# Kernel optimization log

Measured on AMD Instinct MI355X. Metric: run time of the kernel, lower is better.

The kernel has to match this reference:

```python
import jax, jax.numpy as jnp
import numpy as np

B, D, H, W = 16, 64, 64, 64
K = 1024


def setup_inputs() -> dict:
    key = jax.random.key(0)
    k1, k2 = jax.random.split(key)
    x = jax.random.normal(k1, (B, D, H, W), dtype=jnp.float32)
    limit = 3.0 ** 0.5
    e_i_ts = jax.random.uniform(k2, (D, K), dtype=jnp.float32, minval=-limit, maxval=limit)
    return {"x": x, "e_i_ts": e_i_ts}


def reference(x, e_i_ts):
    b, d, h, w = x.shape
    # [B,H,W,D] -> [N,D]
    flat_x = jnp.transpose(x, (0, 2, 3, 1)).reshape(-1, d)
    distances = (
        jnp.sum(flat_x * flat_x, axis=1, keepdims=True)
        - 2.0 * (flat_x @ e_i_ts)
        + jnp.sum(e_i_ts * e_i_ts, axis=0, keepdims=True)
    )
    encoding_indices = jnp.argmin(distances, axis=1)  # [N]
    reshaped_indices = encoding_indices.reshape(b, h, w)
    # codebook gather: e_i_ts.T is [K,D]
    quantized = jnp.take(e_i_ts.T, reshaped_indices, axis=0)  # [B,H,W,D]
    quantized_x = jnp.transpose(quantized, (0, 3, 1, 2))  # [B,D,H,W]

    dictionary_loss = jnp.mean((jax.lax.stop_gradient(x) - quantized_x) ** 2)
    commitment_loss = jnp.mean((x - jax.lax.stop_gradient(quantized_x)) ** 2)
    # straight-through estimator
    quantized_x = x + jax.lax.stop_gradient(quantized_x - x)
    return quantized_x, dictionary_loss, commitment_loss, encoding_indices.reshape(b, -1)
```

## Files before the change

### kernel.cpp

```cpp
#include <hip/hip_runtime.h>

#define DD 64
#define KK 1024
#define NPTS 65536
#define TOTAL 4194304

#define OFF_L1 4194304
#define OFF_L2 4194305
#define OFF_IDX 4194306

#define WS_ENH_F 64
#define WS_EHT_BYTE 65536
#define WS_ELT_BYTE (65536 + 131072)

#define MARGIN_S 0.008f

typedef __attribute__((ext_vector_type(8))) short short8;
typedef __attribute__((ext_vector_type(4))) float f32x4;

__device__ __forceinline__ unsigned short bf16_rne(float f) {
    unsigned b = __float_as_uint(f);
    return (unsigned short)((b + 0x7FFFu + ((b >> 16) & 1u)) >> 16);
}
__device__ __forceinline__ float bf16_to_f(unsigned short h) {
    return __uint_as_float(((unsigned)h) << 16);
}
__device__ __forceinline__ unsigned umax(unsigned a, unsigned b) { return a > b ? a : b; }
__device__ __forceinline__ unsigned umin(unsigned a, unsigned b) { return a < b ? a : b; }
__device__ __forceinline__ void gld_lds16(const void* g, void* l) {
    __builtin_amdgcn_global_load_lds(
        (const __attribute__((address_space(1))) void*)g,
        (__attribute__((address_space(3))) void*)l, 16, 0, 0);
}
__device__ __forceinline__ int swz(int r, int d) {
    return ((d & ~7) ^ ((r & 7) << 3)) | (d & 7);
}

__global__ __launch_bounds__(256) void prep_kernel(const float* __restrict__ e,
                                                   float* __restrict__ enh,
                                                   unsigned short* __restrict__ ehT,
                                                   unsigned short* __restrict__ elT,
                                                   float* __restrict__ sum,
                                                   unsigned* __restrict__ tick) {
    __shared__ unsigned short tH[64 * 64];
    __shared__ unsigned short tL[64 * 64];
    __shared__ float ps[4 * 64];
    const int tid = threadIdx.x, wave = tid >> 6, lane = tid & 63;
    if (blockIdx.x == 0 && tid == 0) { *sum = 0.f; *tick = 0u; }
    const int k = blockIdx.x * 64 + lane;
    float s2 = 0.f;
    short8 hh[2], ll[2];
#pragma unroll
    for (int g = 0; g < 2; ++g)
#pragma unroll
        for (int j = 0; j < 8; ++j) {
            const int d = wave * 16 + g * 8 + j;
            const float v = e[d * KK + k];
            const unsigned short h = bf16_rne(v);
            hh[g][j] = (short)h;
            ll[g][j] = (short)bf16_rne(v - bf16_to_f(h));
            s2 = fmaf(v, v, s2);
        }
    ps[wave * 64 + lane] = s2;
#pragma unroll
    for (int g = 0; g < 2; ++g) {
        const int pos = lane * 64 + ((wave * 16 + g * 8) ^ ((k & 7) << 3));
        *(short8*)(tH + pos) = hh[g];
        *(short8*)(tL + pos) = ll[g];
    }
    __syncthreads();
    if (wave == 0) {
        const float t = ps[lane] + ps[64 + lane] + ps[128 + lane] + ps[192 + lane];
        enh[k] = 512.0f - 0.5f * t;
    }
    {
        const short8* srcH = (const short8*)tH;
        const short8* srcL = (const short8*)tL;
        short8* dstH = (short8*)(ehT + blockIdx.x * 64 * 64);
        short8* dstL = (short8*)(elT + blockIdx.x * 64 * 64);
        dstH[tid * 2]     = srcH[tid * 2];
        dstH[tid * 2 + 1] = srcH[tid * 2 + 1];
        dstL[tid * 2]     = srcL[tid * 2];
        dstL[tid * 2 + 1] = srcL[tid * 2 + 1];
    }
}

__global__ __launch_bounds__(256) void vq_gemm(const float* __restrict__ x,
                                               const float* __restrict__ e,
                                               const float* __restrict__ enh,
                                               const unsigned short* __restrict__ ehT,
                                               const unsigned short* __restrict__ elT,
                                               float* __restrict__ out,
                                               float* __restrict__ sum,
                                               unsigned* __restrict__ tick) {
    __shared__ __align__(16) char ebuf[2 * 16384];

    unsigned short* xbh = (unsigned short*)ebuf;
    unsigned short* xbl = (unsigned short*)(ebuf + 16384);
    int*   ks  = (int*)ebuf;
    float* xp  = (float*)(ks + 128);
    int*   rl  = (int*)(xp + 64);
    int*   rn  = rl + 128;
    float* rv  = (float*)(rn + 1);
    int*   ri  = (int*)(rv + 4);
    float* red = (float*)(ri + 4);

    const int tid = threadIdx.x;
    const int wave = tid >> 6, lane = tid & 63;
    const int n0 = blockIdx.x * 128;
    const int b = n0 >> 12;
    const int hw0 = n0 & 4095;

    const char* ehTb = (const char*)ehT;
    const char* elTb = (const char*)elT;
    const int lofs = wave * 1024 + lane * 16;

    {
        const int p = tid & 127, dg = tid >> 7;
        const float* xs = x + ((b * DD + dg * 32) << 12) + hw0 + p;
        float xv[32];
#pragma unroll
        for (int s = 0; s < 32; ++s) xv[s] = xs[s << 12];
#pragma unroll
        for (int g = 0; g < 4; ++g) {
            short8 hh, ll;
#pragma unroll
            for (int j = 0; j < 8; ++j) {
                const float f = xv[g * 8 + j];
                const unsigned short h = bf16_rne(f);
                hh[j] = (short)h;
                ll[j] = (short)bf16_rne(f - bf16_to_f(h));
            }
            const int d0 = dg * 32 + g * 8;
            const int pos = p * 64 + (d0 ^ ((p & 7) << 3));
            *(short8*)(xbh + pos) = hh;
            *(short8*)(xbl + pos) = ll;
        }
    }
    __syncthreads();

    const int ln15 = lane & 15, q8 = (lane >> 4) * 8;
    const int wp = wave * 32;

    short8 ah[2][2], al[2][2];
#pragma unroll
    for (int rf = 0; rf < 2; ++rf)
#pragma unroll
        for (int kc = 0; kc < 2; ++kc) {
            const int pp = wp + rf * 16 + ln15;
            const int pos = pp * 64 + ((kc * 32 + q8) ^ ((pp & 7) << 3));
            ah[rf][kc] = *(const short8*)(xbh + pos);
            al[rf][kc] = *(const short8*)(xbl + pos);
        }
    __syncthreads();

    {
        char* db = ebuf;
        gld_lds16(ehTb + lofs,        db + wave * 1024);
        gld_lds16(ehTb + 4096 + lofs, db + 4096 + wave * 1024);
        gld_lds16(elTb + lofs,        db + 8192 + wave * 1024);
        gld_lds16(elTb + 4096 + lofs, db + 12288 + wave * 1024);
    }

    unsigned v1u[8], v2u[8];
#pragma unroll
    for (int r = 0; r < 8; ++r) { v1u[r] = 0u; v2u[r] = 0u; }

    for (int kt = 0; kt < 16; ++kt) {
        __syncthreads();
        if (kt < 15) {
            const int nkt = kt + 1;
            char* db = ebuf + (nkt & 1) * 16384;
            const char* sH = ehTb + nkt * 8192 + lofs;
            const char* sL = elTb + nkt * 8192 + lofs;
            gld_lds16(sH,        db + wave * 1024);
            gld_lds16(sH + 4096, db + 4096 + wave * 1024);
            gld_lds16(sL,        db + 8192 + wave * 1024);
            gld_lds16(sL + 4096, db + 12288 + wave * 1024);
        }
        const unsigned short* ebH = (const unsigned short*)(ebuf + (kt & 1) * 16384);
        const unsigned short* ebL = ebH + 4096;

        f32x4 acc[2][4];
#pragma unroll
        for (int cf = 0; cf < 4; ++cf) {
            const float ec = enh[kt * 64 + cf * 16 + ln15];
#pragma unroll
            for (int rf = 0; rf < 2; ++rf)
                acc[rf][cf] = (f32x4){ec, ec, ec, ec};
        }

#pragma unroll
        for (int kc = 0; kc < 2; ++kc) {
            short8 bh[4], bl[4];
#pragma unroll
            for (int cf = 0; cf < 4; ++cf) {
                const int c = cf * 16 + ln15;
                const int pos = c * 64 + ((kc * 32 + q8) ^ ((c & 7) << 3));
                bh[cf] = *(const short8*)(ebH + pos);
                bl[cf] = *(const short8*)(ebL + pos);
            }
#pragma unroll
            for (int rf = 0; rf < 2; ++rf)
#pragma unroll
                for (int cf = 0; cf < 4; ++cf) {
                    acc[rf][cf] = __builtin_amdgcn_mfma_f32_16x16x32_bf16(al[rf][kc], bh[cf], acc[rf][cf], 0, 0, 0);
                    acc[rf][cf] = __builtin_amdgcn_mfma_f32_16x16x32_bf16(ah[rf][kc], bl[cf], acc[rf][cf], 0, 0, 0);
                    acc[rf][cf] = __builtin_amdgcn_mfma_f32_16x16x32_bf16(ah[rf][kc], bh[cf], acc[rf][cf], 0, 0, 0);
                }
        }

#pragma unroll
        for (int rf = 0; rf < 2; ++rf)
#pragma unroll
            for (int reg = 0; reg < 4; ++reg) {
                const int r = rf * 4 + reg;
                const unsigned k0 = (__float_as_uint(acc[rf][0][reg]) | 63u) ^ (unsigned)(kt * 4 + 0);
                const unsigned k1 = (__float_as_uint(acc[rf][1][reg]) | 63u) ^ (unsigned)(kt * 4 + 1);
                const unsigned k2 = (__float_as_uint(acc[rf][2][reg]) | 63u) ^ (unsigned)(kt * 4 + 2);
                const unsigned k3 = (__float_as_uint(acc[rf][3][reg]) | 63u) ^ (unsigned)(kt * 4 + 3);
                unsigned a = umax(k0, k1), bb = umin(k0, k1);
                v2u[r] = umax(umax(v2u[r], umin(v1u[r], a)), bb);
                v1u[r] = umax(v1u[r], a);
                a = umax(k2, k3); bb = umin(k2, k3);
                v2u[r] = umax(umax(v2u[r], umin(v1u[r], a)), bb);
                v1u[r] = umax(v1u[r], a);
            }
    }

    __syncthreads();
    if (tid == 0) *rn = 0;
    __syncthreads();

#pragma unroll
    for (int r = 0; r < 8; ++r) {
        const unsigned c6 = 63u - (v1u[r] & 63u);
        int col = (int)(c6 >> 2) * 64 + (int)(c6 & 3) * 16 + ln15;
        float val = __uint_as_float(v1u[r] & ~63u);
        float sec = __uint_as_float(v2u[r] & ~63u);
#pragma unroll
        for (int msk = 1; msk < 16; msk <<= 1) {
            const float ov = __shfl_xor(val, msk);
            const int oc = __shfl_xor(col, msk);
            const float os = __shfl_xor(sec, msk);
            sec = fmaxf(fmaxf(sec, os), fminf(val, ov));
            const bool t = (ov > val) || (ov == val && oc < col);
            val = t ? ov : val;
            col = t ? oc : col;
        }
        if (ln15 == 0) {
            const int qq = lane >> 4;
            const int pt = wp + (r >> 2) * 16 + qq * 4 + (r & 3);
            ks[pt] = col;
            if (val - sec < MARGIN_S) {
                const int w = atomicAdd(rn, 1);
                rl[w] = pt;
            }
        }
    }
    __syncthreads();

    const int lcnt = *rn;
    for (int it = 0; it < lcnt; ++it) {
        const int pr = rl[it];
        if (tid < 64) xp[tid] = x[((b * DD + tid) << 12) + hw0 + pr];
        __syncthreads();
        float d0 = 0.f, d1 = 0.f, d2 = 0.f, d3 = 0.f;
#pragma unroll 8
        for (int dd = 0; dd < DD; ++dd) {
            const float xd = xp[dd];
            const float4 ev = *(const float4*)(e + dd * KK + tid * 4);
            d0 = fmaf(xd, ev.x, d0);
            d1 = fmaf(xd, ev.y, d1);
            d2 = fmaf(xd, ev.z, d2);
            d3 = fmaf(xd, ev.w, d3);
        }
        const float4 ea = *(const float4*)(enh + tid * 4);
        float bs = d0 + ea.x;
        int bi2 = tid * 4;
        if (d1 + ea.y > bs) { bs = d1 + ea.y; bi2 = tid * 4 + 1; }
        if (d2 + ea.z > bs) { bs = d2 + ea.z; bi2 = tid * 4 + 2; }
        if (d3 + ea.w > bs) { bs = d3 + ea.w; bi2 = tid * 4 + 3; }
#pragma unroll
        for (int m = 1; m < 64; m <<= 1) {
            const float ov = __shfl_xor(bs, m, 64);
            const int oi = __shfl_xor(bi2, m, 64);
            if (ov > bs || (ov == bs && oi < bi2)) { bs = ov; bi2 = oi; }
        }
        if (lane == 0) { rv[wave] = bs; ri[wave] = bi2; }
        __syncthreads();
        if (tid == 0) {
            float gs = rv[0];
            int gi = ri[0];
#pragma unroll
            for (int t2 = 1; t2 < 4; ++t2)
                if (rv[t2] > gs || (rv[t2] == gs && ri[t2] < gi)) { gs = rv[t2]; gi = ri[t2]; }
            ks[pr] = gi;
        }
        __syncthreads();
    }

    if (tid < 128) out[OFF_IDX + n0 + tid] = (float)ks[tid];

    {
        const int pe = tid & 127, dh = tid >> 7;
        const int kp = ks[pe];
        float lacc = 0.f;
#pragma unroll
        for (int s = 0; s < 32; ++s) {
            const int d = dh * 32 + s;
            const float qv = e[d * KK + kp];
            const float xv = x[((b * DD + d) << 12) + hw0 + pe];
            out[((b * DD + d) << 12) + hw0 + pe] = qv;
            const float df = xv - qv;
            lacc = fmaf(df, df, lacc);
        }
#pragma unroll
        for (int off = 32; off > 0; off >>= 1) lacc += __shfl_down(lacc, off, 64);
        if (lane == 0) red[wave] = lacc;
    }
    __syncthreads();
    if (tid == 0) {
        atomicAdd(sum, red[0] + red[1] + red[2] + red[3]);
        __threadfence();
        const unsigned old = atomicAdd(tick, 1u);
        if (old == (unsigned)(gridDim.x - 1)) {
            const float s = atomicAdd(sum, 0.0f);
            const float m = s * (1.0f / (float)TOTAL);
            out[OFF_L1] = m;
            out[OFF_L2] = m;
        }
    }
}

extern "C" void kernel_launch(void* const* d_in, const int* in_sizes, int n_in,
                              void* d_out, int out_size, void* d_ws, size_t ws_size,
                              hipStream_t stream) {
    const float* x = (const float*)d_in[0];
    const float* e = (const float*)d_in[1];
    float* out = (float*)d_out;

    float* sum = (float*)d_ws;
    unsigned* tick = (unsigned*)d_ws + 2;
    float* enh = (float*)d_ws + WS_ENH_F;
    unsigned short* ehT = (unsigned short*)((char*)d_ws + WS_EHT_BYTE);
    unsigned short* elT = (unsigned short*)((char*)d_ws + WS_ELT_BYTE);

    prep_kernel<<<KK / 64, 256, 0, stream>>>(e, enh, ehT, elT, sum, tick);
    vq_gemm<<<NPTS / 128, 256, 0, stream>>>(x, e, enh, ehT, elT, out, sum, tick);
}
```

Measured before the change: 125.5 us.

## Split VQ GEMM into two launches with a triple-buffered per-wave codebook pipeline

The single 512-block launch becomes two 256-block launches. The first half of the points runs the original kernel. The second half runs a new variant where each wave streams its own codebook tiles into a three-slot LDS ring with async global-to-LDS loads and explicit vmcnt waits, and the codebook norms are cached in LDS. The aim is to overlap codebook loads with MFMA work. The cost is an extra kernel launch and serialization between the halves, and the completion counter now uses a fixed total of 512 blocks.

```diff
diff --git a/kernel.cpp b/kernel.cpp
--- a/kernel.cpp
+++ b/kernel.cpp
@@ -4,6 +4,7 @@
 #define KK 1024
 #define NPTS 65536
 #define TOTAL 4194304
+#define NBLK_TOTAL 512
 
 #define OFF_L1 4194304
 #define OFF_L2 4194305
@@ -85,14 +86,15 @@
     }
 }
 
-__global__ __launch_bounds__(256) void vq_gemm(const float* __restrict__ x,
-                                               const float* __restrict__ e,
-                                               const float* __restrict__ enh,
-                                               const unsigned short* __restrict__ ehT,
-                                               const unsigned short* __restrict__ elT,
-                                               float* __restrict__ out,
-                                               float* __restrict__ sum,
-                                               unsigned* __restrict__ tick) {
+
+__global__ __launch_bounds__(256) void vq_gemm_a(const float* __restrict__ x,
+                                                 const float* __restrict__ e,
+                                                 const float* __restrict__ enh,
+                                                 const unsigned short* __restrict__ ehT,
+                                                 const unsigned short* __restrict__ elT,
+                                                 float* __restrict__ out,
+                                                 float* __restrict__ sum,
+                                                 unsigned* __restrict__ tick) {
     __shared__ __align__(16) char ebuf[2 * 16384];
 
     unsigned short* xbh = (unsigned short*)ebuf;
@@ -324,7 +326,247 @@
         atomicAdd(sum, red[0] + red[1] + red[2] + red[3]);
         __threadfence();
         const unsigned old = atomicAdd(tick, 1u);
-        if (old == (unsigned)(gridDim.x - 1)) {
+        if (old == (unsigned)(NBLK_TOTAL - 1)) {
+            const float s = atomicAdd(sum, 0.0f);
+            const float m = s * (1.0f / (float)TOTAL);
+            out[OFF_L1] = m;
+            out[OFF_L2] = m;
+        }
+    }
+}
+
+__global__ __launch_bounds__(256) void vq_gemm_b(const float* __restrict__ x,
+                                                 const float* __restrict__ e,
+                                                 const float* __restrict__ enh,
+                                                 const unsigned short* __restrict__ ehT,
+                                                 const unsigned short* __restrict__ elT,
+                                                 float* __restrict__ out,
+                                                 float* __restrict__ sum,
+                                                 unsigned* __restrict__ tick) {
+    __shared__ __align__(16) char ebuf[4 * 12288];
+    __shared__ float enh_lds[1024];
+
+    unsigned short* xbh = (unsigned short*)ebuf;
+    unsigned short* xbl = (unsigned short*)(ebuf + 16384);
+    int*   ks  = (int*)ebuf;
+    float* xp  = (float*)(ks + 128);
+    int*   rl  = (int*)(xp + 64);
+    int*   rn  = rl + 128;
+    float* rv  = (float*)(rn + 1);
+    int*   ri  = (int*)(rv + 4);
+    float* red = (float*)(ri + 4);
+
+    const int tid = threadIdx.x;
+    const int wave = tid >> 6, lane = tid & 63;
+    const int n0 = (blockIdx.x + 256) * 128;
+    const int b = n0 >> 12;
+    const int hw0 = n0 & 4095;
+
+    const char* ehTb = (const char*)ehT;
+    const char* elTb = (const char*)elT;
+
+    *(float4*)(enh_lds + tid * 4) = *(const float4*)(enh + tid * 4);
+
+    {
+        const int p = tid & 127, dg = tid >> 7;
+        const float* xs = x + ((b * DD + dg * 32) << 12) + hw0 + p;
+        float xv[32];
+#pragma unroll
+        for (int s = 0; s < 32; ++s) xv[s] = xs[s << 12];
+#pragma unroll
+        for (int g = 0; g < 4; ++g) {
+            short8 hh, ll;
+#pragma unroll
+            for (int j = 0; j < 8; ++j) {
+                const float f = xv[g * 8 + j];
+                const unsigned short h = bf16_rne(f);
+                hh[j] = (short)h;
+                ll[j] = (short)bf16_rne(f - bf16_to_f(h));
+            }
+            const int d0 = dg * 32 + g * 8;
+            const int pos = p * 64 + (d0 ^ ((p & 7) << 3));
+            *(short8*)(xbh + pos) = hh;
+            *(short8*)(xbl + pos) = ll;
+        }
+    }
+    __syncthreads();
+
+    const int ln15 = lane & 15, q8 = (lane >> 4) * 8;
+    const int wp = wave * 32;
+
+    short8 ah[2][2], al[2][2];
+#pragma unroll
+    for (int rf = 0; rf < 2; ++rf)
+#pragma unroll
+        for (int kc = 0; kc < 2; ++kc) {
+            const int pp = wp + rf * 16 + ln15;
+            const int pos = pp * 64 + ((kc * 32 + q8) ^ ((pp & 7) << 3));
+            ah[rf][kc] = *(const short8*)(xbh + pos);
+            al[rf][kc] = *(const short8*)(xbl + pos);
+        }
+    __syncthreads();
+
+    char* wbuf = ebuf + wave * 12288;
+    char* r0 = wbuf;
+    char* r1 = wbuf + 4096;
+    char* r2 = wbuf + 8192;
+    const char* sHb = ehTb + lane * 16;
+    const char* sLb = elTb + lane * 16;
+
+#define ISSUE_B(t, dst)                                        \
+    {                                                          \
+        const char* sH = sHb + (t) * 2048;                     \
+        const char* sL = sLb + (t) * 2048;                     \
+        gld_lds16(sH,        (dst));                           \
+        gld_lds16(sH + 1024, (dst) + 1024);                    \
+        gld_lds16(sL,        (dst) + 2048);                    \
+        gld_lds16(sL + 1024, (dst) + 3072);                    \
+    }
+
+    ISSUE_B(0, r0);
+    ISSUE_B(1, r1);
+
+    unsigned v1u[8], v2u[8];
+#pragma unroll
+    for (int r = 0; r < 8; ++r) { v1u[r] = 0u; v2u[r] = 0u; }
+
+    for (int t = 0; t < 64; ++t) {
+        if (t < 63) asm volatile("s_waitcnt vmcnt(4)" ::: "memory");
+        else        asm volatile("s_waitcnt vmcnt(0)" ::: "memory");
+        if (t < 62) ISSUE_B(t + 2, r2);
+
+        const unsigned short* tbH = (const unsigned short*)r0;
+        const unsigned short* tbL = tbH + 1024;
+
+        const float ec = enh_lds[t * 16 + ln15];
+        f32x4 acc[2];
+        acc[0] = (f32x4){ec, ec, ec, ec};
+        acc[1] = acc[0];
+
+#pragma unroll
+        for (int kc = 0; kc < 2; ++kc) {
+            const int pos = ln15 * 64 + ((kc * 32 + q8) ^ ((ln15 & 7) << 3));
+            const short8 bh = *(const short8*)(tbH + pos);
+            const short8 bl = *(const short8*)(tbL + pos);
+#pragma unroll
+            for (int rf = 0; rf < 2; ++rf) {
+                acc[rf] = __builtin_amdgcn_mfma_f32_16x16x32_bf16(al[rf][kc], bh, acc[rf], 0, 0, 0);
+                acc[rf] = __builtin_amdgcn_mfma_f32_16x16x32_bf16(ah[rf][kc], bl, acc[rf], 0, 0, 0);
+                acc[rf] = __builtin_amdgcn_mfma_f32_16x16x32_bf16(ah[rf][kc], bh, acc[rf], 0, 0, 0);
+            }
+        }
+
+#pragma unroll
+        for (int rf = 0; rf < 2; ++rf)
+#pragma unroll
+            for (int reg = 0; reg < 4; ++reg) {
+                const int r = rf * 4 + reg;
+                const unsigned k0 = (__float_as_uint(acc[rf][reg]) | 63u) ^ (unsigned)t;
+                v2u[r] = umax(v2u[r], umin(v1u[r], k0));
+                v1u[r] = umax(v1u[r], k0);
+            }
+
+        char* tmp = r0; r0 = r1; r1 = r2; r2 = tmp;
+    }
+#undef ISSUE_B
+
+    __syncthreads();
+    if (tid == 0) *rn = 0;
+    __syncthreads();
+
+#pragma unroll
+    for (int r = 0; r < 8; ++r) {
+        const unsigned c6 = 63u - (v1u[r] & 63u);
+        int col = (int)c6 * 16 + ln15;
+        float val = __uint_as_float(v1u[r] & ~63u);
+        float sec = __uint_as_float(v2u[r] & ~63u);
+#pragma unroll
+        for (int msk = 1; msk < 16; msk <<= 1) {
+            const float ov = __shfl_xor(val, msk);
+            const int oc = __shfl_xor(col, msk);
+            const float os = __shfl_xor(sec, msk);
+            sec = fmaxf(fmaxf(sec, os), fminf(val, ov));
+            const bool t = (ov > val) || (ov == val && oc < col);
+            val = t ? ov : val;
+            col = t ? oc : col;
+        }
+        if (ln15 == 0) {
+            const int qq = lane >> 4;
+            const int pt = wp + (r >> 2) * 16 + qq * 4 + (r & 3);
+            ks[pt] = col;
+            if (val - sec < MARGIN_S) {
+                const int w = atomicAdd(rn, 1);
+                rl[w] = pt;
+            }
+        }
+    }
+    __syncthreads();
+
+    const int lcnt = *rn;
+    for (int it = 0; it < lcnt; ++it) {
+        const int pr = rl[it];
+        if (tid < 64) xp[tid] = x[((b * DD + tid) << 12) + hw0 + pr];
+        __syncthreads();
+        float d0 = 0.f, d1 = 0.f, d2 = 0.f, d3 = 0.f;
+#pragma unroll 8
+        for (int dd = 0; dd < DD; ++dd) {
+            const float xd = xp[dd];
+            const float4 ev = *(const float4*)(e + dd * KK + tid * 4);
+            d0 = fmaf(xd, ev.x, d0);
+            d1 = fmaf(xd, ev.y, d1);
+            d2 = fmaf(xd, ev.z, d2);
+            d3 = fmaf(xd, ev.w, d3);
+        }
+        const float4 ea = *(const float4*)(enh + tid * 4);
+        float bs = d0 + ea.x;
+        int bi2 = tid * 4;
+        if (d1 + ea.y > bs) { bs = d1 + ea.y; bi2 = tid * 4 + 1; }
+        if (d2 + ea.z > bs) { bs = d2 + ea.z; bi2 = tid * 4 + 2; }
+        if (d3 + ea.w > bs) { bs = d3 + ea.w; bi2 = tid * 4 + 3; }
+#pragma unroll
+        for (int m = 1; m < 64; m <<= 1) {
+            const float ov = __shfl_xor(bs, m, 64);
+            const int oi = __shfl_xor(bi2, m, 64);
+            if (ov > bs || (ov == bs && oi < bi2)) { bs = ov; bi2 = oi; }
+        }
+        if (lane == 0) { rv[wave] = bs; ri[wave] = bi2; }
+        __syncthreads();
+        if (tid == 0) {
+            float gs = rv[0];
+            int gi = ri[0];
+#pragma unroll
+            for (int t2 = 1; t2 < 4; ++t2)
+                if (rv[t2] > gs || (rv[t2] == gs && ri[t2] < gi)) { gs = rv[t2]; gi = ri[t2]; }
+            ks[pr] = gi;
+        }
+        __syncthreads();
+    }
+
+    if (tid < 128) out[OFF_IDX + n0 + tid] = (float)ks[tid];
+
+    {
+        const int pe = tid & 127, dh = tid >> 7;
+        const int kp = ks[pe];
+        float lacc = 0.f;
+#pragma unroll
+        for (int s = 0; s < 32; ++s) {
+            const int d = dh * 32 + s;
+            const float qv = e[d * KK + kp];
+            const float xv = x[((b * DD + d) << 12) + hw0 + pe];
+            out[((b * DD + d) << 12) + hw0 + pe] = qv;
+            const float df = xv - qv;
+            lacc = fmaf(df, df, lacc);
+        }
+#pragma unroll
+        for (int off = 32; off > 0; off >>= 1) lacc += __shfl_down(lacc, off, 64);
+        if (lane == 0) red[wave] = lacc;
+    }
+    __syncthreads();
+    if (tid == 0) {
+        atomicAdd(sum, red[0] + red[1] + red[2] + red[3]);
+        __threadfence();
+        const unsigned old = atomicAdd(tick, 1u);
+        if (old == (unsigned)(NBLK_TOTAL - 1)) {
             const float s = atomicAdd(sum, 0.0f);
             const float m = s * (1.0f / (float)TOTAL);
             out[OFF_L1] = m;
@@ -347,5 +589,6 @@
     unsigned short* elT = (unsigned short*)((char*)d_ws + WS_ELT_BYTE);
 
     prep_kernel<<<KK / 64, 256, 0, stream>>>(e, enh, ehT, elT, sum, tick);
-    vq_gemm<<<NPTS / 128, 256, 0, stream>>>(x, e, enh, ehT, elT, out, sum, tick);
-}
+    vq_gemm_a<<<256, 256, 0, stream>>>(x, e, enh, ehT, elT, out, sum, tick);
+    vq_gemm_b<<<256, 256, 0, stream>>>(x, e, enh, ehT, elT, out, sum, tick);
+}
```

Result: slower. 156.8 us (+24.9%).

## Double block threads to 512 so each wave owns 16 points, cache enh in LDS

Applied to the files above, without the earlier changes.

The GEMM block now runs 8 waves over the same 128 points, so each wave handles one 16-row fragment instead of two. This halves per-thread accumulator and top-2 state, and the codebook tile loads are split so each wave copies half of one table. The enh bias vector is staged once into shared memory instead of being read from global memory on every tile. The fallback path masks to 256 threads and the reductions are widened to 8 waves. The trade-off is less reuse of each B fragment per wave, plus more LDS use and more threads per barrier.

```diff
diff --git a/kernel.cpp b/kernel.cpp
--- a/kernel.cpp
+++ b/kernel.cpp
@@ -4,6 +4,7 @@
 #define KK 1024
 #define NPTS 65536
 #define TOTAL 4194304
+#define NBLK_TOTAL 512
 
 #define OFF_L1 4194304
 #define OFF_L2 4194305
@@ -85,7 +86,7 @@
     }
 }
 
-__global__ __launch_bounds__(256) void vq_gemm(const float* __restrict__ x,
+__global__ __launch_bounds__(512) void vq_gemm(const float* __restrict__ x,
                                                const float* __restrict__ e,
                                                const float* __restrict__ enh,
                                                const unsigned short* __restrict__ ehT,
@@ -94,6 +95,7 @@
                                                float* __restrict__ sum,
                                                unsigned* __restrict__ tick) {
     __shared__ __align__(16) char ebuf[2 * 16384];
+    __shared__ float enh_lds[1024];
 
     unsigned short* xbh = (unsigned short*)ebuf;
     unsigned short* xbl = (unsigned short*)(ebuf + 16384);
@@ -102,8 +104,8 @@
     int*   rl  = (int*)(xp + 64);
     int*   rn  = rl + 128;
     float* rv  = (float*)(rn + 1);
-    int*   ri  = (int*)(rv + 4);
-    float* red = (float*)(ri + 4);
+    int*   ri  = (int*)(rv + 8);
+    float* red = (float*)(ri + 8);
 
     const int tid = threadIdx.x;
     const int wave = tid >> 6, lane = tid & 63;
@@ -113,16 +115,17 @@
 
     const char* ehTb = (const char*)ehT;
     const char* elTb = (const char*)elT;
-    const int lofs = wave * 1024 + lane * 16;
+
+    *(float2*)(enh_lds + tid * 2) = *(const float2*)(enh + tid * 2);
 
     {
         const int p = tid & 127, dg = tid >> 7;
-        const float* xs = x + ((b * DD + dg * 32) << 12) + hw0 + p;
-        float xv[32];
-#pragma unroll
-        for (int s = 0; s < 32; ++s) xv[s] = xs[s << 12];
-#pragma unroll
-        for (int g = 0; g < 4; ++g) {
+        const float* xs = x + ((b * DD + dg * 16) << 12) + hw0 + p;
+        float xv[16];
+#pragma unroll
+        for (int s = 0; s < 16; ++s) xv[s] = xs[s << 12];
+#pragma unroll
+        for (int g = 0; g < 2; ++g) {
             short8 hh, ll;
 #pragma unroll
             for (int j = 0; j < 8; ++j) {
@@ -131,7 +134,7 @@
                 hh[j] = (short)h;
                 ll[j] = (short)bf16_rne(f - bf16_to_f(h));
             }
-            const int d0 = dg * 32 + g * 8;
+            const int d0 = dg * 16 + g * 8;
             const int pos = p * 64 + (d0 ^ ((p & 7) << 3));
             *(short8*)(xbh + pos) = hh;
             *(short8*)(xbl + pos) = ll;
@@ -140,54 +143,49 @@
     __syncthreads();
 
     const int ln15 = lane & 15, q8 = (lane >> 4) * 8;
-    const int wp = wave * 32;
-
-    short8 ah[2][2], al[2][2];
-#pragma unroll
-    for (int rf = 0; rf < 2; ++rf)
-#pragma unroll
-        for (int kc = 0; kc < 2; ++kc) {
-            const int pp = wp + rf * 16 + ln15;
-            const int pos = pp * 64 + ((kc * 32 + q8) ^ ((pp & 7) << 3));
-            ah[rf][kc] = *(const short8*)(xbh + pos);
-            al[rf][kc] = *(const short8*)(xbl + pos);
-        }
-    __syncthreads();
+    const int wp = wave * 16;
+
+    short8 ah[2], al[2];
+#pragma unroll
+    for (int kc = 0; kc < 2; ++kc) {
+        const int pp = wp + ln15;
+        const int pos = pp * 64 + ((kc * 32 + q8) ^ ((pp & 7) << 3));
+        ah[kc] = *(const short8*)(xbh + pos);
+        al[kc] = *(const short8*)(xbl + pos);
+    }
+    __syncthreads();
+
+    const int wsel = (wave < 4) ? wave : (wave - 4);
+    const char* srcTab = (wave < 4) ? ehTb : elTb;
+    const int dofs = ((wave < 4) ? 0 : 8192) + wsel * 2048;
 
     {
-        char* db = ebuf;
-        gld_lds16(ehTb + lofs,        db + wave * 1024);
-        gld_lds16(ehTb + 4096 + lofs, db + 4096 + wave * 1024);
-        gld_lds16(elTb + lofs,        db + 8192 + wave * 1024);
-        gld_lds16(elTb + 4096 + lofs, db + 12288 + wave * 1024);
-    }
-
-    unsigned v1u[8], v2u[8];
-#pragma unroll
-    for (int r = 0; r < 8; ++r) { v1u[r] = 0u; v2u[r] = 0u; }
+        const char* sb = srcTab + wsel * 2048 + lane * 16;
+        gld_lds16(sb,        ebuf + dofs);
+        gld_lds16(sb + 1024, ebuf + dofs + 1024);
+    }
+
+    unsigned v1u[4], v2u[4];
+#pragma unroll
+    for (int r = 0; r < 4; ++r) { v1u[r] = 0u; v2u[r] = 0u; }
 
     for (int kt = 0; kt < 16; ++kt) {
         __syncthreads();
         if (kt < 15) {
             const int nkt = kt + 1;
             char* db = ebuf + (nkt & 1) * 16384;
-            const char* sH = ehTb + nkt * 8192 + lofs;
-            const char* sL = elTb + nkt * 8192 + lofs;
-            gld_lds16(sH,        db + wave * 1024);
-            gld_lds16(sH + 4096, db + 4096 + wave * 1024);
-            gld_lds16(sL,        db + 8192 + wave * 1024);
-            gld_lds16(sL + 4096, db + 12288 + wave * 1024);
+            const char* sb = srcTab + nkt * 8192 + wsel * 2048 + lane * 16;
+            gld_lds16(sb,        db + dofs);
+            gld_lds16(sb + 1024, db + dofs + 1024);
         }
         const unsigned short* ebH = (const unsigned short*)(ebuf + (kt & 1) * 16384);
         const unsigned short* ebL = ebH + 4096;
 
-        f32x4 acc[2][4];
+        f32x4 acc[4];
 #pragma unroll
         for (int cf = 0; cf < 4; ++cf) {
-            const float ec = enh[kt * 64 + cf * 16 + ln15];
-#pragma unroll
-            for (int rf = 0; rf < 2; ++rf)
-                acc[rf][cf] = (f32x4){ec, ec, ec, ec};
+            const float ec = enh_lds[kt * 64 + cf * 16 + ln15];
+            acc[cf] = (f32x4){ec, ec, ec, ec};
         }
 
 #pragma unroll
@@ -201,31 +199,26 @@
                 bl[cf] = *(const short8*)(ebL + pos);
             }
 #pragma unroll
-            for (int rf = 0; rf < 2; ++rf)
-#pragma unroll
-                for (int cf = 0; cf < 4; ++cf) {
-                    acc[rf][cf] = __builtin_amdgcn_mfma_f32_16x16x32_bf16(al[rf][kc], bh[cf], acc[rf][cf], 0, 0, 0);
-                    acc[rf][cf] = __builtin_amdgcn_mfma_f32_16x16x32_bf16(ah[rf][kc], bl[cf], acc[rf][cf], 0, 0, 0);
-                    acc[rf][cf] = __builtin_amdgcn_mfma_f32_16x16x32_bf16(ah[rf][kc], bh[cf], acc[rf][cf], 0, 0, 0);
-                }
-        }
-
-#pragma unroll
-        for (int rf = 0; rf < 2; ++rf)
-#pragma unroll
-            for (int reg = 0; reg < 4; ++reg) {
-                const int r = rf * 4 + reg;
-                const unsigned k0 = (__float_as_uint(acc[rf][0][reg]) | 63u) ^ (unsigned)(kt * 4 + 0);
-                const unsigned k1 = (__float_as_uint(acc[rf][1][reg]) | 63u) ^ (unsigned)(kt * 4 + 1);
-                const unsigned k2 = (__float_as_uint(acc[rf][2][reg]) | 63u) ^ (unsigned)(kt * 4 + 2);
-                const unsigned k3 = (__float_as_uint(acc[rf][3][reg]) | 63u) ^ (unsigned)(kt * 4 + 3);
-                unsigned a = umax(k0, k1), bb = umin(k0, k1);
-                v2u[r] = umax(umax(v2u[r], umin(v1u[r], a)), bb);
-                v1u[r] = umax(v1u[r], a);
-                a = umax(k2, k3); bb = umin(k2, k3);
-                v2u[r] = umax(umax(v2u[r], umin(v1u[r], a)), bb);
-                v1u[r] = umax(v1u[r], a);
-            }
+            for (int cf = 0; cf < 4; ++cf) {
+                acc[cf] = __builtin_amdgcn_mfma_f32_16x16x32_bf16(al[kc], bh[cf], acc[cf], 0, 0, 0);
+                acc[cf] = __builtin_amdgcn_mfma_f32_16x16x32_bf16(ah[kc], bl[cf], acc[cf], 0, 0, 0);
+                acc[cf] = __builtin_amdgcn_mfma_f32_16x16x32_bf16(ah[kc], bh[cf], acc[cf], 0, 0, 0);
+            }
+        }
+
+#pragma unroll
+        for (int reg = 0; reg < 4; ++reg) {
+            const unsigned k0 = (__float_as_uint(acc[0][reg]) | 63u) ^ (unsigned)(kt * 4 + 0);
+            const unsigned k1 = (__float_as_uint(acc[1][reg]) | 63u) ^ (unsigned)(kt * 4 + 1);
+            const unsigned k2 = (__float_as_uint(acc[2][reg]) | 63u) ^ (unsigned)(kt * 4 + 2);
+            const unsigned k3 = (__float_as_uint(acc[3][reg]) | 63u) ^ (unsigned)(kt * 4 + 3);
+            unsigned a = umax(k0, k1), bb = umin(k0, k1);
+            v2u[reg] = umax(umax(v2u[reg], umin(v1u[reg], a)), bb);
+            v1u[reg] = umax(v1u[reg], a);
+            a = umax(k2, k3); bb = umin(k2, k3);
+            v2u[reg] = umax(umax(v2u[reg], umin(v1u[reg], a)), bb);
+            v1u[reg] = umax(v1u[reg], a);
+        }
     }
 
     __syncthreads();
@@ -233,7 +226,7 @@
     __syncthreads();
 
 #pragma unroll
-    for (int r = 0; r < 8; ++r) {
+    for (int r = 0; r < 4; ++r) {
         const unsigned c6 = 63u - (v1u[r] & 63u);
         int col = (int)(c6 >> 2) * 64 + (int)(c6 & 3) * 16 + ln15;
         float val = __uint_as_float(v1u[r] & ~63u);
@@ -250,7 +243,7 @@
         }
         if (ln15 == 0) {
             const int qq = lane >> 4;
-            const int pt = wp + (r >> 2) * 16 + qq * 4 + (r & 3);
+            const int pt = wp + qq * 4 + r;
             ks[pt] = col;
             if (val - sec < MARGIN_S) {
                 const int w = atomicAdd(rn, 1);
@@ -265,22 +258,26 @@
         const int pr = rl[it];
         if (tid < 64) xp[tid] = x[((b * DD + tid) << 12) + hw0 + pr];
         __syncthreads();
-        float d0 = 0.f, d1 = 0.f, d2 = 0.f, d3 = 0.f;
+        float bs = -3.4e38f;
+        int bi2 = 0;
+        if (tid < 256) {
+            float d0 = 0.f, d1 = 0.f, d2 = 0.f, d3 = 0.f;
 #pragma unroll 8
-        for (int dd = 0; dd < DD; ++dd) {
-            const float xd = xp[dd];
-            const float4 ev = *(const float4*)(e + dd * KK + tid * 4);
-            d0 = fmaf(xd, ev.x, d0);
-            d1 = fmaf(xd, ev.y, d1);
-            d2 = fmaf(xd, ev.z, d2);
-            d3 = fmaf(xd, ev.w, d3);
-        }
-        const float4 ea = *(const float4*)(enh + tid * 4);
-        float bs = d0 + ea.x;
-        int bi2 = tid * 4;
-        if (d1 + ea.y > bs) { bs = d1 + ea.y; bi2 = tid * 4 + 1; }
-        if (d2 + ea.z > bs) { bs = d2 + ea.z; bi2 = tid * 4 + 2; }
-        if (d3 + ea.w > bs) { bs = d3 + ea.w; bi2 = tid * 4 + 3; }
+            for (int dd = 0; dd < DD; ++dd) {
+                const float xd = xp[dd];
+                const float4 ev = *(const float4*)(e + dd * KK + tid * 4);
+                d0 = fmaf(xd, ev.x, d0);
+                d1 = fmaf(xd, ev.y, d1);
+                d2 = fmaf(xd, ev.z, d2);
+                d3 = fmaf(xd, ev.w, d3);
+            }
+            const float4 ea = *(const float4*)(enh + tid * 4);
+            bs = d0 + ea.x;
+            bi2 = tid * 4;
+            if (d1 + ea.y > bs) { bs = d1 + ea.y; bi2 = tid * 4 + 1; }
+            if (d2 + ea.z > bs) { bs = d2 + ea.z; bi2 = tid * 4 + 2; }
+            if (d3 + ea.w > bs) { bs = d3 + ea.w; bi2 = tid * 4 + 3; }
+        }
 #pragma unroll
         for (int m = 1; m < 64; m <<= 1) {
             const float ov = __shfl_xor(bs, m, 64);
@@ -293,7 +290,7 @@
             float gs = rv[0];
             int gi = ri[0];
 #pragma unroll
-            for (int t2 = 1; t2 < 4; ++t2)
+            for (int t2 = 1; t2 < 8; ++t2)
                 if (rv[t2] > gs || (rv[t2] == gs && ri[t2] < gi)) { gs = rv[t2]; gi = ri[t2]; }
             ks[pr] = gi;
         }
@@ -307,8 +304,8 @@
         const int kp = ks[pe];
         float lacc = 0.f;
 #pragma unroll
-        for (int s = 0; s < 32; ++s) {
-            const int d = dh * 32 + s;
+        for (int s = 0; s < 16; ++s) {
+            const int d = dh * 16 + s;
             const float qv = e[d * KK + kp];
             const float xv = x[((b * DD + d) << 12) + hw0 + pe];
             out[((b * DD + d) << 12) + hw0 + pe] = qv;
@@ -321,10 +318,13 @@
     }
     __syncthreads();
     if (tid == 0) {
-        atomicAdd(sum, red[0] + red[1] + red[2] + red[3]);
+        float bsum = red[0];
+#pragma unroll
+        for (int w2 = 1; w2 < 8; ++w2) bsum += red[w2];
+        atomicAdd(sum, bsum);
         __threadfence();
         const unsigned old = atomicAdd(tick, 1u);
-        if (old == (unsigned)(gridDim.x - 1)) {
+        if (old == (unsigned)(NBLK_TOTAL - 1)) {
             const float s = atomicAdd(sum, 0.0f);
             const float m = s * (1.0f / (float)TOTAL);
             out[OFF_L1] = m;
@@ -347,5 +347,5 @@
     unsigned short* elT = (unsigned short*)((char*)d_ws + WS_ELT_BYTE);
 
     prep_kernel<<<KK / 64, 256, 0, stream>>>(e, enh, ehT, elT, sum, tick);
-    vq_gemm<<<NPTS / 128, 256, 0, stream>>>(x, e, enh, ehT, elT, out, sum, tick);
-}
+    vq_gemm<<<NPTS / 128, 512, 0, stream>>>(x, e, enh, ehT, elT, out, sum, tick);
+}
```

Result: faster. 122.2 us (-2.6%).
